# Kernel optimization log

Measured on AMD Instinct MI355X. Metric: run time of the kernel, lower is better.

Reference implementation:

```python
import jax, jax.numpy as jnp
import numpy as np

B, S, D, V, N_BLOCKS = 4096, 128, 9, 5, 4


def _pos_encoding(seq_len, dim):
    pos = jnp.arange(seq_len, dtype=jnp.float32)[:, None]
    d = jnp.arange(dim)[None, :]
    angle = pos / jnp.power(10000.0, (2.0 * (d // 2)) / dim).astype(jnp.float32)
    return jnp.where(d % 2 == 0, jnp.sin(angle), jnp.cos(angle))  # [S, D]


def setup_inputs() -> dict:
    key = jax.random.key(0)
    ks = jax.random.split(key, 10)
    sc = 1.0 / np.sqrt(D)
    return {
        "tokens": jax.random.randint(ks[0], (B, S), 0, V),
        "emb": jax.random.normal(ks[1], (V, D), jnp.float32),
        "Wq": jax.random.normal(ks[2], (N_BLOCKS, D, D), jnp.float32) * sc,
        "bq": jax.random.normal(ks[3], (N_BLOCKS, D), jnp.float32) * sc,
        "Wk": jax.random.normal(ks[4], (N_BLOCKS, D, D), jnp.float32) * sc,
        "bk": jax.random.normal(ks[5], (N_BLOCKS, D), jnp.float32) * sc,
        "Wv": jax.random.normal(ks[6], (N_BLOCKS, D, D), jnp.float32) * sc,
        "bv": jax.random.normal(ks[7], (N_BLOCKS, D), jnp.float32) * sc,
        "Wout": jax.random.normal(ks[8], (V, D), jnp.float32) * sc,
        "bout": jax.random.normal(ks[9], (V,), jnp.float32) * sc,
    }


def reference(tokens, emb, Wq, bq, Wk, bk, Wv, bv, Wout, bout):
    seq_len = tokens.shape[1]
    x = emb[tokens] + _pos_encoding(S, D)[:seq_len]  # [B, S, D]
    scale = 1.0 / jnp.sqrt(jnp.asarray(D, x.dtype))
    for i in range(N_BLOCKS):
        # torch Linear: y = x @ W.T + b
        Q = jnp.einsum('bsd,ed->bse', x, Wq[i]) + bq[i]
        K = jnp.einsum('bsd,ed->bse', x, Wk[i]) + bk[i]
        Vv = jnp.einsum('bsd,ed->bse', x, Wv[i]) + bv[i]
        scores = jnp.einsum('bqd,bkd->bqk', Q, K) * scale  # [B, S, S]
        probs = jax.nn.softmax(scores, axis=-1)
        x = jnp.einsum('bqk,bkd->bqd', probs, Vv)
    logits = jnp.einsum('bsd,vd->bsv', x, Wout) + bout  # [B, S, V]
    return jax.nn.log_softmax(logits, axis=-1)
```

## Files before the change

kernel.cpp:

```cpp
#include <hip/hip_runtime.h>
#include <math.h>

constexpr int Bn = 4096;
constexpr int Sn = 128;
constexpr int Dn = 9;
constexpr int Vn = 5;
constexpr int NBn = 4;

typedef float f4 __attribute__((ext_vector_type(4)));
typedef _Float16 h8 __attribute__((ext_vector_type(8)));
typedef __fp16   h2 __attribute__((ext_vector_type(2)));
typedef unsigned u4v __attribute__((ext_vector_type(4)));
typedef short s4v __attribute__((ext_vector_type(4)));

constexpr int WS_PE = 384;

constexpr int KF_OFF = 0;
constexpr int QF_OFF = 10240;
constexpr int VF_OFF = 20480;
constexpr int XB_OFF = 24832;
constexpr int SMEM_BYTES = 30976;

static __device__ __forceinline__ void split_hl(const float* v, _Float16* H, _Float16* L) {
    #pragma unroll
    for (int i = 0; i < 9; ++i) {
        _Float16 h = (_Float16)v[i];
        H[i] = h;
        L[i] = (_Float16)(v[i] - (float)h);
    }
}

static __device__ __forceinline__ unsigned pk(_Float16 a, _Float16 b) {
    h2 t; t.x = (__fp16)a; t.y = (__fp16)b;
    return __builtin_bit_cast(unsigned, t);
}

static __device__ __forceinline__ void store_row32(short* rowp,
        const _Float16* X, const _Float16* Y, const _Float16* Z,
        _Float16 T0, _Float16 T1) {
    const _Float16 z0 = (_Float16)0.0f;
    u4v w0 = (u4v){ pk(X[0],X[1]), pk(X[2],X[3]), pk(X[4],X[5]), pk(X[6],X[7]) };
    u4v w1 = (u4v){ pk(X[8],Y[0]), pk(Y[1],Y[2]), pk(Y[3],Y[4]), pk(Y[5],Y[6]) };
    u4v w2 = (u4v){ pk(Y[7],Y[8]), pk(Z[0],Z[1]), pk(Z[2],Z[3]), pk(Z[4],Z[5]) };
    u4v w3 = (u4v){ pk(Z[6],Z[7]), pk(Z[8],T0),   pk(T1,z0),     0u            };
    u4v* qp = (u4v*)rowp;
    qp[0] = w0; qp[1] = w1; qp[2] = w2; qp[3] = w3;
}

static __device__ __forceinline__ h8 read_quad(const short* base, int row, int quad) {
    return *(const h8*)(base + row * 40 + quad * 8);
}

__global__ void prep_kernel(const float* __restrict__ Wq, const float* __restrict__ bq,
                            const float* __restrict__ Wk, float* __restrict__ ws)
{
    const float qs = (1.0f / 3.0f) * 1.44269504f;
    const int idx = blockIdx.x * 256 + threadIdx.x;
    if (idx < 360) {
        const int it = idx / 90, j = idx % 90;
        const float* wq = Wq + it * 81;
        const float* wk = Wk + it * 81;
        float acc = 0.0f;
        if (j < 81) {
            const int e = j / 9, d = j % 9;
            #pragma unroll
            for (int f = 0; f < 9; ++f) acc = fmaf(wk[f * 9 + e], wq[f * 9 + d], acc);
        } else {
            const int d = j - 81;
            const float* bqp = bq + it * 9;
            #pragma unroll
            for (int f = 0; f < 9; ++f) acc = fmaf(wk[f * 9 + d], bqp[f], acc);
        }
        ws[it * 96 + j] = acc * qs;
    } else if (idx < 360 + Sn * Dn) {
        const int j = idx - 360;
        const int r = j / 9, d = j % 9;
        const float inv_freq[Dn] = {
            1.0f, 1.0f, 0.1291549665f, 0.1291549665f, 0.0166810054f,
            0.0166810054f, 0.0021544347f, 0.0021544347f, 0.0002782559f };
        const float a = (float)r * inv_freq[d];
        ws[WS_PE + j] = (d & 1) ? cosf(a) : sinf(a);
    }
}

__global__ __launch_bounds__(256, 4) void bert_kernel(
    const int*   __restrict__ tokens,
    const float* __restrict__ emb,
    const float* __restrict__ Wv, const float* __restrict__ bv,
    const float* __restrict__ Wout, const float* __restrict__ bout,
    const float* __restrict__ wsp,
    float*       __restrict__ out)
{
    __shared__ __align__(16) char smem[SMEM_BYTES];
    short* KF = (short*)(smem + KF_OFF);
    short* QF = (short*)(smem + QF_OFF);
    short* VF = (short*)(smem + VF_OFF);
    float* XB = (float*)(smem + XB_OFF);

    const int b   = blockIdx.x;
    const int tid = threadIdx.x;
    const int t   = tid & 63;
    const int w   = tid >> 6;
    const int col = t & 15;
    const int g   = t >> 4;
    const bool lowhalf = tid < 128;
    const int r = lowhalf ? tid : tid - 128;
    const float* MP = wsp;
    const float* PE = wsp + WS_PE;

    if (lowhalf) {
        const int tok = tokens[b * Sn + r];
        float xr[9];
        #pragma unroll
        for (int d = 0; d < Dn; ++d)
            xr[d] = emb[tok * Dn + d] + PE[r * 9 + d];
        f4* xp = (f4*)&XB[r * 12];
        xp[0] = (f4){xr[0], xr[1], xr[2], xr[3]};
        xp[1] = (f4){xr[4], xr[5], xr[6], xr[7]};
        xp[2] = (f4){xr[8], 0.0f, 0.0f, 0.0f};
    } else {
        VF[9 * 136 + r] = (short)0x3C00;
    }
    __syncthreads();

    #pragma unroll 1
    for (int it = 0; it < NBn; ++it) {
        {
            const f4* xp = (const f4*)&XB[r * 12];
            f4 a0 = xp[0], a1 = xp[1], a2 = xp[2];
            float x[9] = {a0.x, a0.y, a0.z, a0.w, a1.x, a1.y, a1.z, a1.w, a2.x};
            const float* wv  = Wv + it * 81;
            const float* bvi = bv + it * 9;
            const float* mp  = MP + it * 96;
            if (lowhalf) {
                float tb = 0.0f;
                #pragma unroll
                for (int d = 0; d < Dn; ++d) tb = fmaf(x[d], mp[81 + d], tb);
                _Float16 H[9], L[9];
                split_hl(x, H, L);
                _Float16 th = (_Float16)tb;
                _Float16 tl = (_Float16)(tb - (float)th);
                store_row32(KF + r * 40, H, H, L, th, tl);
                #pragma unroll
                for (int e = 0; e < 8; ++e) {
                    float av = bvi[e];
                    #pragma unroll
                    for (int d = 0; d < Dn; ++d) av = fmaf(x[d], wv[e * 9 + d], av);
                    VF[e * 136 + r] = __builtin_bit_cast(short, (_Float16)av);
                }
            } else {
                float y[9];
                #pragma unroll
                for (int e = 0; e < Dn; ++e) {
                    float a = 0.0f;
                    #pragma unroll
                    for (int d = 0; d < Dn; ++d) a = fmaf(x[d], mp[e * 9 + d], a);
                    y[e] = a;
                }
                _Float16 H[9], L[9];
                split_hl(y, H, L);
                store_row32(QF + r * 40, H, L, H,
                            (_Float16)1.0f, (_Float16)1.0f);
                float av = bvi[8];
                #pragma unroll
                for (int d = 0; d < Dn; ++d) av = fmaf(x[d], wv[8 * 9 + d], av);
                VF[8 * 136 + r] = __builtin_bit_cast(short, (_Float16)av);
            }
        }
        __syncthreads();

        h8 kfr[8];
        #pragma unroll
        for (int kt = 0; kt < 8; ++kt)
            kfr[kt] = read_quad(KF, kt * 16 + col, g);

        h8 vf[4];
        #pragma unroll
        for (int s = 0; s < 4; ++s) {
            const short* p0 = VF + col * 136 + 32 * s + 4 * g;
            s4v va = *(const s4v*)p0;
            s4v vb = *(const s4v*)(p0 + 16);
            vf[s] = __builtin_bit_cast(h8,
                __builtin_shufflevector(va, vb, 0, 1, 2, 3, 4, 5, 6, 7));
        }

        #pragma unroll
        for (int ti = 0; ti < 2; ++ti) {
            const int qt = 2 * w + ti;
            const int q  = qt * 16 + col;
            h8 bq3 = read_quad(QF, q, g);

            f4 acc[8];
            #pragma unroll
            for (int kt = 0; kt < 8; ++kt)
                acc[kt] = __builtin_amdgcn_mfma_f32_16x16x32_f16(kfr[kt], bq3, (f4)(0.0f), 0, 0, 0);

            #pragma unroll
            for (int kt = 0; kt < 8; ++kt)
                #pragma unroll
                for (int rr = 0; rr < 4; ++rr)
                    acc[kt][rr] = __builtin_amdgcn_exp2f(acc[kt][rr]);

            f4 oac = (f4)(0.0f);
            #pragma unroll
            for (int s = 0; s < 4; ++s) {
                u4v up = (u4v){
                    __builtin_bit_cast(unsigned, __builtin_amdgcn_cvt_pkrtz(acc[2*s][0],   acc[2*s][1])),
                    __builtin_bit_cast(unsigned, __builtin_amdgcn_cvt_pkrtz(acc[2*s][2],   acc[2*s][3])),
                    __builtin_bit_cast(unsigned, __builtin_amdgcn_cvt_pkrtz(acc[2*s+1][0], acc[2*s+1][1])),
                    __builtin_bit_cast(unsigned, __builtin_amdgcn_cvt_pkrtz(acc[2*s+1][2], acc[2*s+1][3])) };
                oac = __builtin_amdgcn_mfma_f32_16x16x32_f16(vf[s], __builtin_bit_cast(h8, up), oac, 0, 0, 0);
            }
            const float sm = __shfl(oac[1], 32 + col);
            const float rl = __builtin_amdgcn_rcpf(sm);
            oac *= rl;
            if (g < 3)
                *(f4*)&XB[q * 12 + g * 4] = oac;
        }
        __syncthreads();
    }

    if (lowhalf) {
        const f4* xp = (const f4*)&XB[r * 12];
        f4 a0 = xp[0], a1 = xp[1], a2 = xp[2];
        float xr[9] = {a0.x, a0.y, a0.z, a0.w, a1.x, a1.y, a1.z, a1.w, a2.x};
        float lg[Vn];
        #pragma unroll
        for (int v = 0; v < Vn; ++v) {
            float a = bout[v];
            #pragma unroll
            for (int d = 0; d < Dn; ++d) a = fmaf(xr[d], Wout[v * Dn + d], a);
            lg[v] = a;
        }
        float mm = lg[0];
        #pragma unroll
        for (int v = 1; v < Vn; ++v) mm = fmaxf(mm, lg[v]);
        float sum = 0.0f;
        #pragma unroll
        for (int v = 0; v < Vn; ++v)
            sum += __builtin_amdgcn_exp2f((lg[v] - mm) * 1.44269504f);
        const float lse = __builtin_amdgcn_logf(sum) * 0.69314718f + mm;
        float* op = out + ((size_t)b * Sn + r) * Vn;
        #pragma unroll
        for (int v = 0; v < Vn; ++v) op[v] = lg[v] - lse;
    }
}

extern "C" void kernel_launch(void* const* d_in, const int* in_sizes, int n_in,
                              void* d_out, int out_size, void* d_ws, size_t ws_size,
                              hipStream_t stream) {
    const int*   tokens = (const int*)  d_in[0];
    const float* emb    = (const float*)d_in[1];
    const float* Wq     = (const float*)d_in[2];
    const float* bq_    = (const float*)d_in[3];
    const float* Wk     = (const float*)d_in[4];
    const float* Wv     = (const float*)d_in[6];
    const float* bv_    = (const float*)d_in[7];
    const float* Wout   = (const float*)d_in[8];
    const float* bout_  = (const float*)d_in[9];
    float* out = (float*)d_out;
    float* ws  = (float*)d_ws;

    prep_kernel<<<dim3(6), dim3(256), 0, stream>>>(Wq, bq_, Wk, ws);
    bert_kernel<<<dim3(Bn), dim3(256), 0, stream>>>(
        tokens, emb, Wv, bv_, Wout, bout_, ws, out);
}
```

Baseline: 128.4 us.

## Compute per-block Q-fold and V projections with MFMA using precomputed fp16 weight fragments

Measured after the change: 128.9 us. No clear change (+0.4%).

```diff
diff --git a/kernel.cpp b/kernel.cpp
--- a/kernel.cpp
+++ b/kernel.cpp
@@ -14,6 +14,7 @@
 typedef short s4v __attribute__((ext_vector_type(4)));
 
 constexpr int WS_PE = 384;
+constexpr int WS_FRAG_BYTES = 6144;
 
 constexpr int KF_OFF = 0;
 constexpr int QF_OFF = 10240;
@@ -21,30 +22,9 @@
 constexpr int XB_OFF = 24832;
 constexpr int SMEM_BYTES = 30976;
 
-static __device__ __forceinline__ void split_hl(const float* v, _Float16* H, _Float16* L) {
-    #pragma unroll
-    for (int i = 0; i < 9; ++i) {
-        _Float16 h = (_Float16)v[i];
-        H[i] = h;
-        L[i] = (_Float16)(v[i] - (float)h);
-    }
-}
-
 static __device__ __forceinline__ unsigned pk(_Float16 a, _Float16 b) {
     h2 t; t.x = (__fp16)a; t.y = (__fp16)b;
     return __builtin_bit_cast(unsigned, t);
-}
-
-static __device__ __forceinline__ void store_row32(short* rowp,
-        const _Float16* X, const _Float16* Y, const _Float16* Z,
-        _Float16 T0, _Float16 T1) {
-    const _Float16 z0 = (_Float16)0.0f;
-    u4v w0 = (u4v){ pk(X[0],X[1]), pk(X[2],X[3]), pk(X[4],X[5]), pk(X[6],X[7]) };
-    u4v w1 = (u4v){ pk(X[8],Y[0]), pk(Y[1],Y[2]), pk(Y[3],Y[4]), pk(Y[5],Y[6]) };
-    u4v w2 = (u4v){ pk(Y[7],Y[8]), pk(Z[0],Z[1]), pk(Z[2],Z[3]), pk(Z[4],Z[5]) };
-    u4v w3 = (u4v){ pk(Z[6],Z[7]), pk(Z[8],T0),   pk(T1,z0),     0u            };
-    u4v* qp = (u4v*)rowp;
-    qp[0] = w0; qp[1] = w1; qp[2] = w2; qp[3] = w3;
 }
 
 static __device__ __forceinline__ h8 read_quad(const short* base, int row, int quad) {
@@ -83,10 +63,36 @@
     }
 }
 
+__global__ void prep2_kernel(const float* __restrict__ Wv, const float* __restrict__ bv,
+                             float* __restrict__ ws)
+{
+    const int idx = blockIdx.x * 256 + threadIdx.x;
+    if (idx >= 4096) return;
+    const int it = idx >> 10, rem = idx & 1023, op = rem >> 9;
+    const int e = (rem >> 5) & 15, s = rem & 31;
+    float v = 0.0f;
+    bool lo = false;
+    if (s < 27) {
+        const int d = (s < 9) ? s : (s < 18 ? s - 9 : s - 18);
+        lo = (s >= 18);
+        if (op == 0) {
+            if (e < 9)       v = ws[it * 96 + e * 9 + d];
+            else if (e == 9) v = ws[it * 96 + 81 + d];
+        } else {
+            if (e < 9)       v = Wv[it * 81 + e * 9 + d];
+        }
+    } else if (op == 1 && e < 9 && s >= 30) {
+        v = bv[it * 9 + e];
+        lo = (s == 31);
+    }
+    const _Float16 h = (_Float16)v;
+    const _Float16 r = lo ? (_Float16)(v - (float)h) : h;
+    ((_Float16*)((char*)ws + WS_FRAG_BYTES))[idx] = r;
+}
+
 __global__ __launch_bounds__(256, 4) void bert_kernel(
     const int*   __restrict__ tokens,
     const float* __restrict__ emb,
-    const float* __restrict__ Wv, const float* __restrict__ bv,
     const float* __restrict__ Wout, const float* __restrict__ bout,
     const float* __restrict__ wsp,
     float*       __restrict__ out)
@@ -100,15 +106,17 @@
     const int b   = blockIdx.x;
     const int tid = threadIdx.x;
     const int t   = tid & 63;
-    const int w   = tid >> 6;
+    const int wv  = tid >> 6;
     const int col = t & 15;
     const int g   = t >> 4;
-    const bool lowhalf = tid < 128;
-    const int r = lowhalf ? tid : tid - 128;
-    const float* MP = wsp;
+    const bool hi = tid >= 128;
+    const int r = tid & 127;
     const float* PE = wsp + WS_PE;
-
-    if (lowhalf) {
+    const _Float16* FB = (const _Float16*)((const char*)wsp + WS_FRAG_BYTES);
+    const _Float16 one = (_Float16)1.0f;
+    const _Float16 z0  = (_Float16)0.0f;
+
+    if (!hi) {
         const int tok = tokens[b * Sn + r];
         float xr[9];
         #pragma unroll
@@ -125,46 +133,73 @@
 
     #pragma unroll 1
     for (int it = 0; it < NBn; ++it) {
+        const _Float16* fb = FB + it * 1024;
+        const h8 aM = *(const h8*)(fb + col * 32 + g * 8);
+        const h8 aV = *(const h8*)(fb + 512 + col * 32 + g * 8);
+
         {
             const f4* xp = (const f4*)&XB[r * 12];
             f4 a0 = xp[0], a1 = xp[1], a2 = xp[2];
             float x[9] = {a0.x, a0.y, a0.z, a0.w, a1.x, a1.y, a1.z, a1.w, a2.x};
-            const float* wv  = Wv + it * 81;
-            const float* bvi = bv + it * 9;
-            const float* mp  = MP + it * 96;
-            if (lowhalf) {
-                float tb = 0.0f;
+            _Float16 H[9];
+            #pragma unroll
+            for (int d = 0; d < Dn; ++d) H[d] = (_Float16)x[d];
+            u4v* qp = (u4v*)(KF + r * 40);
+            if (!hi) {
+                const _Float16 l7 = (_Float16)(x[7] - (float)H[7]);
+                const _Float16 l8 = (_Float16)(x[8] - (float)H[8]);
+                qp[0] = (u4v){ pk(H[0],H[1]), pk(H[2],H[3]), pk(H[4],H[5]), pk(H[6],H[7]) };
+                qp[2] = (u4v){ pk(l7,l8),     pk(H[0],H[1]), pk(H[2],H[3]), pk(H[4],H[5]) };
+            } else {
+                _Float16 l[7];
                 #pragma unroll
-                for (int d = 0; d < Dn; ++d) tb = fmaf(x[d], mp[81 + d], tb);
-                _Float16 H[9], L[9];
-                split_hl(x, H, L);
-                _Float16 th = (_Float16)tb;
-                _Float16 tl = (_Float16)(tb - (float)th);
-                store_row32(KF + r * 40, H, H, L, th, tl);
+                for (int d = 0; d < 7; ++d) l[d] = (_Float16)(x[d] - (float)H[d]);
+                qp[1] = (u4v){ pk(H[8],l[0]), pk(l[1],l[2]), pk(l[3],l[4]), pk(l[5],l[6]) };
+                qp[3] = (u4v){ pk(H[6],H[7]), pk(H[8],z0), 0u, pk(one,one) };
+            }
+        }
+        __syncthreads();
+
+        #pragma unroll
+        for (int sub = 0; sub < 2; ++sub) {
+            const int xrow = (2 * wv + sub) * 16 + col;
+            h8 bx = read_quad(KF, xrow, g);
+            f4 yD = __builtin_amdgcn_mfma_f32_16x16x32_f16(aM, bx, (f4)(0.0f), 0, 0, 0);
+            f4 vD = __builtin_amdgcn_mfma_f32_16x16x32_f16(aV, bx, (f4)(0.0f), 0, 0, 0);
+            if (g < 3) *(f4*)&XB[xrow * 12 + g * 4] = yD;
+            #pragma unroll
+            for (int rr = 0; rr < 4; ++rr) {
+                const int e = 4 * g + rr;
+                if (e < 9)
+                    VF[e * 136 + xrow] = __builtin_bit_cast(short, (_Float16)vD[rr]);
+            }
+        }
+        __syncthreads();
+
+        {
+            const f4* xp = (const f4*)&XB[r * 12];
+            f4 b0 = xp[0], b1 = xp[1], b2 = xp[2];
+            float y[9] = {b0.x, b0.y, b0.z, b0.w, b1.x, b1.y, b1.z, b1.w, b2.x};
+            const float tb = b2.y;
+            _Float16 H[9];
+            #pragma unroll
+            for (int e = 0; e < Dn; ++e) H[e] = (_Float16)y[e];
+            u4v* qq = (u4v*)(QF + r * 40);
+            if (!hi) {
+                _Float16 l[6];
                 #pragma unroll
-                for (int e = 0; e < 8; ++e) {
-                    float av = bvi[e];
-                    #pragma unroll
-                    for (int d = 0; d < Dn; ++d) av = fmaf(x[d], wv[e * 9 + d], av);
-                    VF[e * 136 + r] = __builtin_bit_cast(short, (_Float16)av);
-                }
+                for (int e = 0; e < 6; ++e) l[e] = (_Float16)(y[e] - (float)H[e]);
+                qq[0] = (u4v){ pk(H[0],H[1]), pk(H[2],H[3]), pk(H[4],H[5]), pk(H[6],H[7]) };
+                qq[2] = (u4v){ pk(H[7],H[8]), pk(l[0],l[1]), pk(l[2],l[3]), pk(l[4],l[5]) };
             } else {
-                float y[9];
-                #pragma unroll
-                for (int e = 0; e < Dn; ++e) {
-                    float a = 0.0f;
-                    #pragma unroll
-                    for (int d = 0; d < Dn; ++d) a = fmaf(x[d], mp[e * 9 + d], a);
-                    y[e] = a;
-                }
-                _Float16 H[9], L[9];
-                split_hl(y, H, L);
-                store_row32(QF + r * 40, H, L, H,
-                            (_Float16)1.0f, (_Float16)1.0f);
-                float av = bvi[8];
-                #pragma unroll
-                for (int d = 0; d < Dn; ++d) av = fmaf(x[d], wv[8 * 9 + d], av);
-                VF[8 * 136 + r] = __builtin_bit_cast(short, (_Float16)av);
+                const _Float16 l6 = (_Float16)(y[6] - (float)H[6]);
+                const _Float16 l7 = (_Float16)(y[7] - (float)H[7]);
+                const _Float16 l8 = (_Float16)(y[8] - (float)H[8]);
+                qq[1] = (u4v){ pk(H[8],H[0]), pk(H[1],H[2]), pk(H[3],H[4]), pk(H[5],H[6]) };
+                qq[3] = (u4v){ pk(l6,l7),     pk(l8,z0),     pk(one,one),   0u };
+                const _Float16 th = (_Float16)tb;
+                const _Float16 tl = (_Float16)(tb - (float)th);
+                ((unsigned*)(KF + r * 40))[14] = pk(th, tl);
             }
         }
         __syncthreads();
@@ -186,7 +221,7 @@
 
         #pragma unroll
         for (int ti = 0; ti < 2; ++ti) {
-            const int qt = 2 * w + ti;
+            const int qt = 2 * wv + ti;
             const int q  = qt * 16 + col;
             h8 bq3 = read_quad(QF, q, g);
 
@@ -220,7 +255,7 @@
         __syncthreads();
     }
 
-    if (lowhalf) {
+    if (!hi) {
         const f4* xp = (const f4*)&XB[r * 12];
         f4 a0 = xp[0], a1 = xp[1], a2 = xp[2];
         float xr[9] = {a0.x, a0.y, a0.z, a0.w, a1.x, a1.y, a1.z, a1.w, a2.x};
@@ -262,6 +297,7 @@
     float* ws  = (float*)d_ws;
 
     prep_kernel<<<dim3(6), dim3(256), 0, stream>>>(Wq, bq_, Wk, ws);
+    prep2_kernel<<<dim3(16), dim3(256), 0, stream>>>(Wv, bv_, ws);
     bert_kernel<<<dim3(Bn), dim3(256), 0, stream>>>(
-        tokens, emb, Wv, bv_, Wout, bout_, ws, out);
-}
+        tokens, emb, Wout, bout_, ws, out);
+}
```
